# Kernel tuning notes

Measured on AMD Instinct MI355X. Metric: run time of the kernel, lower is better.

Reference implementation:

```python
import jax, jax.numpy as jnp
import numpy as np

W, B, C, H = 1600, 4, 1, 900
DENSITY = 0.03          # fraction of valid radar returns per column
DEPTH_MAX = 80.0        # metric depth range


def setup_inputs() -> dict:
    key = jax.random.key(0)
    k1, k2, k3 = jax.random.split(key, 3)
    radar_depth = jax.random.uniform(k1, (W, B, C, H, 1), jnp.float32) * DEPTH_MAX + 1.0
    radar_mask = jax.random.uniform(k2, (W, B, C, H, 1), jnp.float32) < DENSITY
    radar_patches = jnp.where(radar_mask, radar_depth, 0.0)
    # dense monocular depth estimate, strictly positive (all 'valid')
    mde_out_patches = jax.random.uniform(k3, (W, B, C, H, 1), jnp.float32) * DEPTH_MAX + 1.0
    return {"radar_patches": radar_patches, "mde_out_patches": mde_out_patches}


def _process_column(radar_col, mde_col):
    """Sequentially place valid radar depths of one (w,b) column.

    radar_col, mde_col: [H] float (channel 0 of the column).
    Returns radar_gt column [H].
    Matches torch loop: for each valid radar y (ascending), pick mde row with
    closest depth (argmin |mde - d|, first index on ties); if that slot is
    already occupied, search outward offsets +1,-1,+2,-2,... for an empty slot;
    if none found, overwrite the best slot.
    """
    h = radar_col.shape[0]
    ys = jnp.arange(h)
    mde_valid = mde_col != 0
    has_mde = jnp.any(mde_valid)
    BIG = jnp.float32(1e30)
    KBIG = 4 * h  # sentinel key for occupied slots

    def step(col, y):
        depth = radar_col[y]
        valid = depth != 0
        # per-point argmin over valid mde depths
        diffs = jnp.where(mde_valid, jnp.abs(mde_col - depth), BIG)
        best_y = jnp.where(has_mde, jnp.argmin(diffs), y)
        # outward collision search as a vectorized argmin over a priority key:
        #   best_y itself -> 0; offset o, +dy before -dy -> 2*o + (dy<0)
        occ = col != 0
        dy = ys - best_y
        key = 2 * jnp.abs(dy) + (dy < 0).astype(jnp.int32)
        key = jnp.where(ys == best_y, 0, key)
        key = jnp.where(occ, KBIG, key)
        final_y = jnp.argmin(key)
        # all slots occupied -> fall back to best_y (torch overwrites there)
        final_y = jnp.where(key[final_y] >= KBIG, best_y, final_y)
        new_col = jnp.where(valid, col.at[final_y].set(depth), col)
        return new_col, None

    col, _ = jax.lax.scan(step, jnp.zeros(h, radar_col.dtype), ys)
    return col


def reference(radar_patches, mde_out_patches):
    # channel 0 only is read/written, as in the torch code
    radar0 = radar_patches[:, :, 0, :, 0]   # [W, B, H]
    mde0 = mde_out_patches[:, :, 0, :, 0]   # [W, B, H]
    cols = jax.vmap(jax.vmap(_process_column))(radar0, mde0)  # [W, B, H]
    w, b, h = cols.shape
    c = radar_patches.shape[2]
    radar_gt = jnp.zeros((b, c, h, w), radar_patches.dtype)
    radar_gt = radar_gt.at[:, 0].set(jnp.transpose(cols, (1, 2, 0)))  # [B, H, W]
    return radar_gt
```

## Files before the change

### kernel.cpp

```cpp
#include <hip/hip_runtime.h>
#include <cstdint>
#include <cstddef>

#define WDIM 1600
#define BDIM 4
#define HDIM 900
#define NV4  225
#define NCHV 4
#define QCAP 96
#define KBIG (4 * HDIM)
#define BW   6

__global__ __launch_bounds__(256) void radar_place_kernel(
    const float* __restrict__ radar, const float* __restrict__ mde,
    float* __restrict__ colout , int direct, float* __restrict__ out)
{
    __shared__ __align__(16) float s_col[4][HDIM];
    __shared__ float s_qd[4][QCAP];
    __shared__ int   s_qy[4][QCAP];

    const int wave = threadIdx.x >> 6;
    const int lane = threadIdx.x & 63;
    const int lane4 = lane << 2;
    const int colid = blockIdx.x * 4 + wave;
    const float4* mde4   = (const float4*)mde   + (long)colid * NV4;
    const float4* radar4 = (const float4*)radar + (long)colid * NV4;

    float* col  = s_col[wave];
    float4* col4 = (float4*)col;
    float* qd   = s_qd[wave];
    int*   qy   = s_qy[wave];

    const unsigned long long below = (1ull << lane) - 1ull;

    float m[16];
    bool hm = false;
    int Q = 0;
#pragma unroll
    for (int c = 0; c < NCHV; ++c) {
        int i4 = c * 64 + lane;
        bool in = (i4 < NV4);
        float4 mv = in ? mde4[i4] : make_float4(0.f, 0.f, 0.f, 0.f);
        m[c * 4 + 0] = (mv.x != 0.f) ? mv.x : 1e30f;
        m[c * 4 + 1] = (mv.y != 0.f) ? mv.y : 1e30f;
        m[c * 4 + 2] = (mv.z != 0.f) ? mv.z : 1e30f;
        m[c * 4 + 3] = (mv.w != 0.f) ? mv.w : 1e30f;
        hm = hm || (mv.x != 0.f) || (mv.y != 0.f) || (mv.z != 0.f) || (mv.w != 0.f);

        if (in) col4[i4] = make_float4(0.f, 0.f, 0.f, 0.f);

        float4 rv = in ? radar4[i4] : make_float4(0.f, 0.f, 0.f, 0.f);
        unsigned long long b0 = __ballot(rv.x != 0.f);
        unsigned long long b1 = __ballot(rv.y != 0.f);
        unsigned long long b2 = __ballot(rv.z != 0.f);
        unsigned long long b3 = __ballot(rv.w != 0.f);
        int pos = Q + __popcll(b0 & below) + __popcll(b1 & below)
                    + __popcll(b2 & below) + __popcll(b3 & below);
        int y0 = i4 * 4;
        if (rv.x != 0.f) { if (pos < QCAP) { qd[pos] = rv.x; qy[pos] = y0;     } pos++; }
        if (rv.y != 0.f) { if (pos < QCAP) { qd[pos] = rv.y; qy[pos] = y0 + 1; } pos++; }
        if (rv.z != 0.f) { if (pos < QCAP) { qd[pos] = rv.z; qy[pos] = y0 + 2; } pos++; }
        if (rv.w != 0.f) { if (pos < QCAP) { qd[pos] = rv.w; qy[pos] = y0 + 3; } pos++; }
        Q += __popcll(b0) + __popcll(b1) + __popcll(b2) + __popcll(b3);
    }
    if (Q > QCAP) Q = QCAP;
    const bool has_mde = (__ballot(hm) != 0ull);

    unsigned occ = (lane >= 33) ? 0xF000u : 0u;

    for (int t = 0; t < Q; t += BW) {
        float d[BW];
#pragma unroll
        for (int i = 0; i < BW; ++i) {
            int idx = (t + i < Q) ? (t + i) : (Q - 1);
            d[i] = qd[idx];
        }
        float bd[BW], bo[BW];
        int bi[BW];
#pragma unroll
        for (int i = 0; i < BW; ++i) { bd[i] = 3.4e38f; bi[i] = 0; }
#pragma unroll
        for (int c = 0; c < NCHV; ++c) {
#pragma unroll
            for (int j = 0; j < 4; ++j) {
                float mm = m[c * 4 + j];
                int yy = c * 256 + lane4 + j;
#pragma unroll
                for (int i = 0; i < BW; ++i) {
                    float af = fabsf(mm - d[i]);
                    if (af < bd[i]) { bd[i] = af; bi[i] = yy; }
                }
            }
        }
#pragma unroll
        for (int i = 0; i < BW; ++i) bo[i] = bd[i];
#pragma unroll
        for (int off = 32; off; off >>= 1)
#pragma unroll
            for (int i = 0; i < BW; ++i)
                bd[i] = fminf(bd[i], __shfl_xor(bd[i], off));
#pragma unroll
        for (int i = 0; i < BW; ++i)
            bi[i] = (bo[i] == bd[i]) ? bi[i] : 0x7fffffff;
#pragma unroll
        for (int off = 32; off; off >>= 1)
#pragma unroll
            for (int i = 0; i < BW; ++i) {
                int v = __shfl_xor(bi[i], off);
                bi[i] = (v < bi[i]) ? v : bi[i];
            }

#pragma unroll
        for (int i = 0; i < BW; ++i) {
            if (t + i < Q) {
                int best;
                if (has_mde) best = __builtin_amdgcn_readfirstlane(bi[i]);
                else         best = __builtin_amdgcn_readfirstlane(qy[t + i]);
                float depth = d[i];
                int bi4 = best >> 2, bj = best & 3;
                int bc = bi4 >> 6, bl = bi4 & 63;
                int bbit = bc * 4 + bj;
                unsigned long long bm = __ballot((occ >> bbit) & 1u);
                int final_y = best;
                if ((bm >> bl) & 1ull) {
                    int bk = 0x7fffffff, bki = 0;
#pragma unroll
                    for (int c = 0; c < NCHV; ++c) {
#pragma unroll
                        for (int j = 0; j < 4; ++j) {
                            int yy = c * 256 + lane4 + j;
                            int o = (occ >> (c * 4 + j)) & 1u;
                            int dy = yy - best;
                            int ad = dy < 0 ? -dy : dy;
                            int key = o ? KBIG : (2 * ad + (dy < 0 ? 1 : 0));
                            if (key < bk) { bk = key; bki = yy; }
                        }
                    }
                    int bko = bk;
#pragma unroll
                    for (int off = 32; off; off >>= 1) {
                        int v = __shfl_xor(bk, off);
                        bk = (v < bk) ? v : bk;
                    }
                    int c2 = (bko == bk) ? bki : 0x7fffffff;
#pragma unroll
                    for (int off = 32; off; off >>= 1) {
                        int v = __shfl_xor(c2, off);
                        c2 = (v < c2) ? v : c2;
                    }
                    int fk = __builtin_amdgcn_readfirstlane(bk);
                    int gi = __builtin_amdgcn_readfirstlane(c2);
                    final_y = (fk >= KBIG) ? best : gi;
                }
                int fi4 = final_y >> 2, fj = final_y & 3;
                int fc = fi4 >> 6, fl = fi4 & 63;
                if (lane == fl) occ |= (1u << (fc * 4 + fj));
                if (lane == 0) col[final_y] = depth;
            }
        }
    }

    if (direct) {
        int w_ = colid >> 2, b_ = colid & 3;
#pragma unroll
        for (int c = 0; c < NCHV; ++c) {
            int i4 = c * 64 + lane;
            if (i4 < NV4) {
                float4 v = col4[i4];
                int y = i4 * 4;
                out[((long)(b_ * HDIM + y + 0)) * WDIM + w_] = v.x;
                out[((long)(b_ * HDIM + y + 1)) * WDIM + w_] = v.y;
                out[((long)(b_ * HDIM + y + 2)) * WDIM + w_] = v.z;
                out[((long)(b_ * HDIM + y + 3)) * WDIM + w_] = v.w;
            }
        }
    } else {
        float4* colout4 = (float4*)colout + (long)colid * NV4;
#pragma unroll
        for (int c = 0; c < NCHV; ++c) {
            int i4 = c * 64 + lane;
            if (i4 < NV4) colout4[i4] = col4[i4];
        }
    }
}

__global__ __launch_bounds__(256) void transpose_kernel(
    const float* __restrict__ colout, float* __restrict__ out)
{
    __shared__ float tile[32][33];
    const int b  = blockIdx.z;
    const int h0 = blockIdx.x * 32;
    const int w0 = blockIdx.y * 32;
    const int tx = threadIdx.x & 31;
    const int ty = threadIdx.x >> 5;
#pragma unroll
    for (int j = 0; j < 4; ++j) {
        int wl = ty + j * 8;
        int w = w0 + wl;
        int h = h0 + tx;
        float v = 0.0f;
        if (h < HDIM && w < WDIM) v = colout[((long)(w * BDIM + b)) * HDIM + h];
        tile[wl][tx] = v;
    }
    __syncthreads();
#pragma unroll
    for (int j = 0; j < 4; ++j) {
        int hl = ty + j * 8;
        int h = h0 + hl;
        int w = w0 + tx;
        if (h < HDIM && w < WDIM)
            out[((long)(b * HDIM + h)) * WDIM + w] = tile[tx][hl];
    }
}

extern "C" void kernel_launch(void* const* d_in, const int* in_sizes, int n_in,
                              void* d_out, int out_size, void* d_ws, size_t ws_size,
                              hipStream_t stream) {
    const float* radar = (const float*)d_in[0];
    const float* mde   = (const float*)d_in[1];
    float* out = (float*)d_out;
    float* ws  = (float*)d_ws;

    const size_t need = (size_t)WDIM * BDIM * HDIM * sizeof(float);
    const int direct = (ws_size < need) ? 1 : 0;

    hipLaunchKernelGGL(radar_place_kernel,
                       dim3(WDIM * BDIM / 4), dim3(256), 0, stream,
                       radar, mde, ws, direct, out);

    if (!direct) {
        dim3 g((HDIM + 31) / 32, WDIM / 32, BDIM);
        hipLaunchKernelGGL(transpose_kernel, g, dim3(256), 0, stream, ws, out);
    }
}
```

Measured before the change: 148.5 us.

## Split argmin and placement phases, fast-path unique argmin, use 2-wave blocks

Restructures the per-column loop into two phases. First, batched argmins are computed and stored to shared memory, with a ballot/popcount fast path that skips the index-min shuffle reduction when only one lane holds the minimum. Second, a separate sequential placement loop reads those results. Blocks shrink from 4 waves to 2 with a launch-bounds occupancy hint, to improve scheduling granularity and occupancy. The split adds shared-memory traffic and an extra loop, and the fast path adds a ballot per item.

Result: slower. 160.4 us (+8.0%).

```diff
diff --git a/kernel.cpp b/kernel.cpp
--- a/kernel.cpp
+++ b/kernel.cpp
@@ -10,26 +10,29 @@
 #define QCAP 96
 #define KBIG (4 * HDIM)
 #define BW   6
-
-__global__ __launch_bounds__(256) void radar_place_kernel(
+#define NWAVE 2
+
+__global__ __launch_bounds__(64 * NWAVE, 8) void radar_place_kernel(
     const float* __restrict__ radar, const float* __restrict__ mde,
     float* __restrict__ colout , int direct, float* __restrict__ out)
 {
-    __shared__ __align__(16) float s_col[4][HDIM];
-    __shared__ float s_qd[4][QCAP];
-    __shared__ int   s_qy[4][QCAP];
+    __shared__ __align__(16) float s_col[NWAVE][HDIM];
+    __shared__ float s_qd[NWAVE][QCAP];
+    __shared__ int   s_qy[NWAVE][QCAP];
+    __shared__ int   s_by[NWAVE][QCAP];
 
     const int wave = threadIdx.x >> 6;
     const int lane = threadIdx.x & 63;
     const int lane4 = lane << 2;
-    const int colid = blockIdx.x * 4 + wave;
+    const int colid = blockIdx.x * NWAVE + wave;
     const float4* mde4   = (const float4*)mde   + (long)colid * NV4;
     const float4* radar4 = (const float4*)radar + (long)colid * NV4;
 
-    float* col  = s_col[wave];
+    float*  col  = s_col[wave];
     float4* col4 = (float4*)col;
-    float* qd   = s_qd[wave];
-    int*   qy   = s_qy[wave];
+    float*  qd   = s_qd[wave];
+    int*    qy   = s_qy[wave];
+    int*    by   = s_by[wave];
 
     const unsigned long long below = (1ull << lane) - 1ull;
 
@@ -66,8 +69,6 @@
     if (Q > QCAP) Q = QCAP;
     const bool has_mde = (__ballot(hm) != 0ull);
 
-    unsigned occ = (lane >= 33) ? 0xF000u : 0u;
-
     for (int t = 0; t < Q; t += BW) {
         float d[BW];
 #pragma unroll
@@ -100,64 +101,66 @@
             for (int i = 0; i < BW; ++i)
                 bd[i] = fminf(bd[i], __shfl_xor(bd[i], off));
 #pragma unroll
-        for (int i = 0; i < BW; ++i)
-            bi[i] = (bo[i] == bd[i]) ? bi[i] : 0x7fffffff;
-#pragma unroll
-        for (int off = 32; off; off >>= 1)
-#pragma unroll
-            for (int i = 0; i < BW; ++i) {
-                int v = __shfl_xor(bi[i], off);
-                bi[i] = (v < bi[i]) ? v : bi[i];
-            }
-
-#pragma unroll
         for (int i = 0; i < BW; ++i) {
-            if (t + i < Q) {
-                int best;
-                if (has_mde) best = __builtin_amdgcn_readfirstlane(bi[i]);
-                else         best = __builtin_amdgcn_readfirstlane(qy[t + i]);
-                float depth = d[i];
-                int bi4 = best >> 2, bj = best & 3;
-                int bc = bi4 >> 6, bl = bi4 & 63;
-                int bbit = bc * 4 + bj;
-                unsigned long long bm = __ballot((occ >> bbit) & 1u);
-                int final_y = best;
-                if ((bm >> bl) & 1ull) {
-                    int bk = 0x7fffffff, bki = 0;
-#pragma unroll
-                    for (int c = 0; c < NCHV; ++c) {
-#pragma unroll
-                        for (int j = 0; j < 4; ++j) {
-                            int yy = c * 256 + lane4 + j;
-                            int o = (occ >> (c * 4 + j)) & 1u;
-                            int dy = yy - best;
-                            int ad = dy < 0 ? -dy : dy;
-                            int key = o ? KBIG : (2 * ad + (dy < 0 ? 1 : 0));
-                            if (key < bk) { bk = key; bki = yy; }
-                        }
-                    }
-                    int bko = bk;
-#pragma unroll
-                    for (int off = 32; off; off >>= 1) {
-                        int v = __shfl_xor(bk, off);
-                        bk = (v < bk) ? v : bk;
-                    }
-                    int c2 = (bko == bk) ? bki : 0x7fffffff;
-#pragma unroll
-                    for (int off = 32; off; off >>= 1) {
-                        int v = __shfl_xor(c2, off);
-                        c2 = (v < c2) ? v : c2;
-                    }
-                    int fk = __builtin_amdgcn_readfirstlane(bk);
-                    int gi = __builtin_amdgcn_readfirstlane(c2);
-                    final_y = (fk >= KBIG) ? best : gi;
+            unsigned long long wm = __ballot(bo[i] == bd[i]);
+            int res;
+            if (__popcll(wm) == 1) {
+                res = __shfl(bi[i], __ffsll(wm) - 1);
+            } else {
+                int c2 = (bo[i] == bd[i]) ? bi[i] : 0x7fffffff;
+#pragma unroll
+                for (int off = 32; off; off >>= 1) {
+                    int v = __shfl_xor(c2, off);
+                    c2 = (v < c2) ? v : c2;
                 }
-                int fi4 = final_y >> 2, fj = final_y & 3;
-                int fc = fi4 >> 6, fl = fi4 & 63;
-                if (lane == fl) occ |= (1u << (fc * 4 + fj));
-                if (lane == 0) col[final_y] = depth;
-            }
-        }
+                res = c2;
+            }
+            if (lane == 0 && t + i < Q) by[t + i] = res;
+        }
+    }
+
+    unsigned occ = (lane >= 33) ? 0xF000u : 0u;
+
+    for (int q = 0; q < Q; ++q) {
+        int best = has_mde ? by[q] : qy[q];
+        float depth = qd[q];
+        int bi4 = best >> 2, bj = best & 3;
+        int bc = bi4 >> 6, bl = bi4 & 63;
+        int bbit = bc * 4 + bj;
+        unsigned long long bm = __ballot((occ >> bbit) & 1u);
+        int final_y = best;
+        if ((bm >> bl) & 1ull) {
+            int bk = 0x7fffffff, bki = 0;
+#pragma unroll
+            for (int c = 0; c < NCHV; ++c) {
+#pragma unroll
+                for (int j = 0; j < 4; ++j) {
+                    int yy = c * 256 + lane4 + j;
+                    int o = (occ >> (c * 4 + j)) & 1u;
+                    int dy = yy - best;
+                    int ad = dy < 0 ? -dy : dy;
+                    int key = o ? KBIG : (2 * ad + (dy < 0 ? 1 : 0));
+                    if (key < bk) { bk = key; bki = yy; }
+                }
+            }
+            int bko = bk;
+#pragma unroll
+            for (int off = 32; off; off >>= 1) {
+                int v = __shfl_xor(bk, off);
+                bk = (v < bk) ? v : bk;
+            }
+            int c2 = (bko == bk) ? bki : 0x7fffffff;
+#pragma unroll
+            for (int off = 32; off; off >>= 1) {
+                int v = __shfl_xor(c2, off);
+                c2 = (v < c2) ? v : c2;
+            }
+            final_y = (bk >= KBIG) ? best : c2;
+        }
+        int fi4 = final_y >> 2, fj = final_y & 3;
+        int fc = fi4 >> 6, fl = fi4 & 63;
+        if (lane == fl) occ |= (1u << (fc * 4 + fj));
+        if (lane == 0) col[final_y] = depth;
     }
 
     if (direct) {
@@ -225,7 +228,7 @@
     const int direct = (ws_size < need) ? 1 : 0;
 
     hipLaunchKernelGGL(radar_place_kernel,
-                       dim3(WDIM * BDIM / 4), dim3(256), 0, stream,
+                       dim3(WDIM * BDIM / NWAVE), dim3(64 * NWAVE), 0, stream,
                        radar, mde, ws, direct, out);
 
     if (!direct) {
```

## Use contiguous 15-row-per-lane MDE layout, DPP min reductions, one-wave blocks

Applied to the files above, without the earlier changes.

Each lane now owns a contiguous block of 15 rows (60 active lanes), loaded through LDS, instead of strided float4 chunks. This cuts the per-lane argmin loop from 16 to 15 elements and lets the winning row be found with a ballot plus ffs instead of a second shuffle reduction. The float min reduction uses DPP row ops and a readlane in place of shfl_xor. Blocks shrink to a single 64-thread wave per column, which adds block count and extra syncthreads in exchange for simpler indexing.

Measured after the change: 137.0 us. 7.8% less time.

```diff
diff --git a/kernel.cpp b/kernel.cpp
--- a/kernel.cpp
+++ b/kernel.cpp
@@ -6,49 +6,47 @@
 #define BDIM 4
 #define HDIM 900
 #define NV4  225
-#define NCHV 4
 #define QCAP 96
 #define KBIG (4 * HDIM)
 #define BW   6
 
-__global__ __launch_bounds__(256) void radar_place_kernel(
+#define DPP_MINF(v, ctrl)                                                  \
+    v = fminf(v, __int_as_float(__builtin_amdgcn_update_dpp(               \
+            __float_as_int(v), __float_as_int(v), ctrl, 0xf, 0xf, false)))
+
+__global__ __launch_bounds__(64) void radar_place_kernel(
     const float* __restrict__ radar, const float* __restrict__ mde,
     float* __restrict__ colout , int direct, float* __restrict__ out)
 {
-    __shared__ __align__(16) float s_col[4][HDIM];
-    __shared__ float s_qd[4][QCAP];
-    __shared__ int   s_qy[4][QCAP];
-
-    const int wave = threadIdx.x >> 6;
-    const int lane = threadIdx.x & 63;
-    const int lane4 = lane << 2;
-    const int colid = blockIdx.x * 4 + wave;
+    __shared__ __align__(16) float s_col[HDIM];
+    __shared__ float s_qd[QCAP];
+    __shared__ int   s_qy[QCAP];
+
+    const int lane = threadIdx.x;
+    const int colid = blockIdx.x;
     const float4* mde4   = (const float4*)mde   + (long)colid * NV4;
     const float4* radar4 = (const float4*)radar + (long)colid * NV4;
-
-    float* col  = s_col[wave];
-    float4* col4 = (float4*)col;
-    float* qd   = s_qd[wave];
-    int*   qy   = s_qy[wave];
+    float4* col4 = (float4*)s_col;
 
     const unsigned long long below = (1ull << lane) - 1ull;
 
-    float m[16];
     bool hm = false;
+#pragma unroll
+    for (int c = 0; c < 4; ++c) {
+        int i4 = c * 64 + lane;
+        if (i4 < NV4) {
+            float4 mv = mde4[i4];
+            hm = hm || (mv.x != 0.f) || (mv.y != 0.f) || (mv.z != 0.f) || (mv.w != 0.f);
+            col4[i4] = mv;
+        }
+    }
+    const bool has_mde = (__ballot(hm) != 0ull);
+
     int Q = 0;
 #pragma unroll
-    for (int c = 0; c < NCHV; ++c) {
+    for (int c = 0; c < 4; ++c) {
         int i4 = c * 64 + lane;
         bool in = (i4 < NV4);
-        float4 mv = in ? mde4[i4] : make_float4(0.f, 0.f, 0.f, 0.f);
-        m[c * 4 + 0] = (mv.x != 0.f) ? mv.x : 1e30f;
-        m[c * 4 + 1] = (mv.y != 0.f) ? mv.y : 1e30f;
-        m[c * 4 + 2] = (mv.z != 0.f) ? mv.z : 1e30f;
-        m[c * 4 + 3] = (mv.w != 0.f) ? mv.w : 1e30f;
-        hm = hm || (mv.x != 0.f) || (mv.y != 0.f) || (mv.z != 0.f) || (mv.w != 0.f);
-
-        if (in) col4[i4] = make_float4(0.f, 0.f, 0.f, 0.f);
-
         float4 rv = in ? radar4[i4] : make_float4(0.f, 0.f, 0.f, 0.f);
         unsigned long long b0 = __ballot(rv.x != 0.f);
         unsigned long long b1 = __ballot(rv.y != 0.f);
@@ -57,113 +55,131 @@
         int pos = Q + __popcll(b0 & below) + __popcll(b1 & below)
                     + __popcll(b2 & below) + __popcll(b3 & below);
         int y0 = i4 * 4;
-        if (rv.x != 0.f) { if (pos < QCAP) { qd[pos] = rv.x; qy[pos] = y0;     } pos++; }
-        if (rv.y != 0.f) { if (pos < QCAP) { qd[pos] = rv.y; qy[pos] = y0 + 1; } pos++; }
-        if (rv.z != 0.f) { if (pos < QCAP) { qd[pos] = rv.z; qy[pos] = y0 + 2; } pos++; }
-        if (rv.w != 0.f) { if (pos < QCAP) { qd[pos] = rv.w; qy[pos] = y0 + 3; } pos++; }
+        if (rv.x != 0.f) { if (pos < QCAP) { s_qd[pos] = rv.x; s_qy[pos] = y0;     } pos++; }
+        if (rv.y != 0.f) { if (pos < QCAP) { s_qd[pos] = rv.y; s_qy[pos] = y0 + 1; } pos++; }
+        if (rv.z != 0.f) { if (pos < QCAP) { s_qd[pos] = rv.z; s_qy[pos] = y0 + 2; } pos++; }
+        if (rv.w != 0.f) { if (pos < QCAP) { s_qd[pos] = rv.w; s_qy[pos] = y0 + 3; } pos++; }
         Q += __popcll(b0) + __popcll(b1) + __popcll(b2) + __popcll(b3);
     }
     if (Q > QCAP) Q = QCAP;
-    const bool has_mde = (__ballot(hm) != 0ull);
-
-    unsigned occ = (lane >= 33) ? 0xF000u : 0u;
+
+    __syncthreads();
+
+    float m[15];
+    if (lane < 60) {
+        int yb = lane * 15;
+#pragma unroll
+        for (int k = 0; k < 15; ++k) {
+            float v = s_col[yb + k];
+            m[k] = (v != 0.f) ? v : 1e30f;
+        }
+    } else {
+#pragma unroll
+        for (int k = 0; k < 15; ++k) m[k] = 1e30f;
+    }
+
+    __syncthreads();
+
+#pragma unroll
+    for (int c = 0; c < 4; ++c) {
+        int i4 = c * 64 + lane;
+        if (i4 < NV4) col4[i4] = make_float4(0.f, 0.f, 0.f, 0.f);
+    }
+
+    unsigned occ = (lane >= 60) ? 0x7FFFu : 0u;
 
     for (int t = 0; t < Q; t += BW) {
         float d[BW];
 #pragma unroll
         for (int i = 0; i < BW; ++i) {
             int idx = (t + i < Q) ? (t + i) : (Q - 1);
-            d[i] = qd[idx];
+            d[i] = s_qd[idx];
         }
         float bd[BW], bo[BW];
-        int bi[BW];
-#pragma unroll
-        for (int i = 0; i < BW; ++i) { bd[i] = 3.4e38f; bi[i] = 0; }
-#pragma unroll
-        for (int c = 0; c < NCHV; ++c) {
-#pragma unroll
-            for (int j = 0; j < 4; ++j) {
-                float mm = m[c * 4 + j];
-                int yy = c * 256 + lane4 + j;
-#pragma unroll
-                for (int i = 0; i < BW; ++i) {
-                    float af = fabsf(mm - d[i]);
-                    if (af < bd[i]) { bd[i] = af; bi[i] = yy; }
-                }
+        int bik[BW];
+#pragma unroll
+        for (int i = 0; i < BW; ++i) { bd[i] = 3.4e38f; bik[i] = 0; }
+#pragma unroll
+        for (int k = 0; k < 15; ++k) {
+            float mm = m[k];
+#pragma unroll
+            for (int i = 0; i < BW; ++i) {
+                float af = fabsf(mm - d[i]);
+                if (af < bd[i]) { bd[i] = af; bik[i] = k; }
             }
         }
 #pragma unroll
         for (int i = 0; i < BW; ++i) bo[i] = bd[i];
 #pragma unroll
-        for (int off = 32; off; off >>= 1)
-#pragma unroll
-            for (int i = 0; i < BW; ++i)
-                bd[i] = fminf(bd[i], __shfl_xor(bd[i], off));
-#pragma unroll
-        for (int i = 0; i < BW; ++i)
-            bi[i] = (bo[i] == bd[i]) ? bi[i] : 0x7fffffff;
-#pragma unroll
-        for (int off = 32; off; off >>= 1)
-#pragma unroll
-            for (int i = 0; i < BW; ++i) {
-                int v = __shfl_xor(bi[i], off);
-                bi[i] = (v < bi[i]) ? v : bi[i];
-            }
+        for (int i = 0; i < BW; ++i) DPP_MINF(bd[i], 0x111);
+#pragma unroll
+        for (int i = 0; i < BW; ++i) DPP_MINF(bd[i], 0x112);
+#pragma unroll
+        for (int i = 0; i < BW; ++i) DPP_MINF(bd[i], 0x114);
+#pragma unroll
+        for (int i = 0; i < BW; ++i) DPP_MINF(bd[i], 0x118);
+#pragma unroll
+        for (int i = 0; i < BW; ++i) DPP_MINF(bd[i], 0x142);
+#pragma unroll
+        for (int i = 0; i < BW; ++i) DPP_MINF(bd[i], 0x143);
 
 #pragma unroll
         for (int i = 0; i < BW; ++i) {
             if (t + i < Q) {
                 int best;
-                if (has_mde) best = __builtin_amdgcn_readfirstlane(bi[i]);
-                else         best = __builtin_amdgcn_readfirstlane(qy[t + i]);
+                if (has_mde) {
+                    float gm = __int_as_float(
+                        __builtin_amdgcn_readlane(__float_as_int(bd[i]), 63));
+                    unsigned long long wm = __ballot(bo[i] == gm);
+                    int win = __ffsll((long long)wm) - 1;
+                    int kst = __shfl(bik[i], win);
+                    best = win * 15 + kst;
+                } else {
+                    best = s_qy[t + i];
+                }
                 float depth = d[i];
-                int bi4 = best >> 2, bj = best & 3;
-                int bc = bi4 >> 6, bl = bi4 & 63;
-                int bbit = bc * 4 + bj;
-                unsigned long long bm = __ballot((occ >> bbit) & 1u);
-                int final_y = best;
+                int sb = __builtin_amdgcn_readfirstlane(best);
+                int bl = sb / 15, bk = sb % 15;
+                unsigned long long bm = __ballot((occ >> bk) & 1u);
+                int final_y = sb;
                 if ((bm >> bl) & 1ull) {
-                    int bk = 0x7fffffff, bki = 0;
-#pragma unroll
-                    for (int c = 0; c < NCHV; ++c) {
-#pragma unroll
-                        for (int j = 0; j < 4; ++j) {
-                            int yy = c * 256 + lane4 + j;
-                            int o = (occ >> (c * 4 + j)) & 1u;
-                            int dy = yy - best;
-                            int ad = dy < 0 ? -dy : dy;
-                            int key = o ? KBIG : (2 * ad + (dy < 0 ? 1 : 0));
-                            if (key < bk) { bk = key; bki = yy; }
-                        }
+                    int ko = 0x7fffffff, kk = 0;
+#pragma unroll
+                    for (int k = 0; k < 15; ++k) {
+                        int yy = lane * 15 + k;
+                        int o = (occ >> k) & 1;
+                        int dy = yy - sb;
+                        int ad = dy < 0 ? -dy : dy;
+                        int key = o ? KBIG : (2 * ad + (dy < 0 ? 1 : 0));
+                        if (key < ko) { ko = key; kk = k; }
                     }
-                    int bko = bk;
+                    int kmin = ko;
 #pragma unroll
                     for (int off = 32; off; off >>= 1) {
-                        int v = __shfl_xor(bk, off);
-                        bk = (v < bk) ? v : bk;
+                        int v = __shfl_xor(kmin, off);
+                        kmin = (v < kmin) ? v : kmin;
                     }
-                    int c2 = (bko == bk) ? bki : 0x7fffffff;
-#pragma unroll
-                    for (int off = 32; off; off >>= 1) {
-                        int v = __shfl_xor(c2, off);
-                        c2 = (v < c2) ? v : c2;
+                    if (kmin < KBIG) {
+                        unsigned long long wm2 = __ballot(ko == kmin);
+                        int w2 = __ffsll((long long)wm2) - 1;
+                        int k2 = __shfl(kk, w2);
+                        final_y = w2 * 15 + k2;
                     }
-                    int fk = __builtin_amdgcn_readfirstlane(bk);
-                    int gi = __builtin_amdgcn_readfirstlane(c2);
-                    final_y = (fk >= KBIG) ? best : gi;
                 }
-                int fi4 = final_y >> 2, fj = final_y & 3;
-                int fc = fi4 >> 6, fl = fi4 & 63;
-                if (lane == fl) occ |= (1u << (fc * 4 + fj));
-                if (lane == 0) col[final_y] = depth;
+                int sf = __builtin_amdgcn_readfirstlane(final_y);
+                int fl = sf / 15, fk = sf % 15;
+                if (lane == fl) occ |= (1u << fk);
+                if (lane == 0) s_col[sf] = depth;
             }
         }
     }
+
+    __syncthreads();
 
     if (direct) {
         int w_ = colid >> 2, b_ = colid & 3;
 #pragma unroll
-        for (int c = 0; c < NCHV; ++c) {
+        for (int c = 0; c < 4; ++c) {
             int i4 = c * 64 + lane;
             if (i4 < NV4) {
                 float4 v = col4[i4];
@@ -177,7 +193,7 @@
     } else {
         float4* colout4 = (float4*)colout + (long)colid * NV4;
 #pragma unroll
-        for (int c = 0; c < NCHV; ++c) {
+        for (int c = 0; c < 4; ++c) {
             int i4 = c * 64 + lane;
             if (i4 < NV4) colout4[i4] = col4[i4];
         }
@@ -225,7 +241,7 @@
     const int direct = (ws_size < need) ? 1 : 0;
 
     hipLaunchKernelGGL(radar_place_kernel,
-                       dim3(WDIM * BDIM / 4), dim3(256), 0, stream,
+                       dim3(WDIM * BDIM), dim3(64), 0, stream,
                        radar, mde, ws, direct, out);
 
     if (!direct) {
```
